# Kernel tuning notes

Hardware: AMD Instinct MI355X
Metric: run time of the kernel (lower is better)

The kernel has to match this reference:

```python
import jax, jax.numpy as jnp
import numpy as np

MESSAGE_PASSES = 3  # constants.message_passes
F_NODE = 64   # hidden_node_features
F_EDGE = 16   # n_edge_features
M_MSG = 64    # message_size
OUT_DIM = 128
B, N = 8, 256
EDGE_DENSITY = 0.1


def setup_inputs() -> dict:
    key = jax.random.key(0)
    ks = jax.random.split(key, 12)
    nodes = jax.random.normal(ks[0], (B, N, F_NODE), dtype=jnp.float32)
    # sparse positive edge features: rand * bernoulli connectivity (avg degree ~ N*density)
    raw = jax.random.uniform(ks[1], (B, N, N, F_EDGE), dtype=jnp.float32)
    conn = (jax.random.uniform(ks[2], (B, N, N)) < EDGE_DENSITY).astype(jnp.float32)
    edges = raw * conn[..., None]
    s = 0.05
    return {
        "nodes": nodes,
        "edges": edges,
        # message MLP: cat(neighbour, edge) -> message_size
        "W_msg": jax.random.normal(ks[3], (F_NODE + F_EDGE, M_MSG), dtype=jnp.float32) * s,
        "b_msg": jnp.zeros((M_MSG,), dtype=jnp.float32),
        # GRU cell (input=message_size, hidden=F_NODE), gates [r|z|n]
        "W_i": jax.random.normal(ks[4], (M_MSG, 3 * F_NODE), dtype=jnp.float32) * s,
        "W_h": jax.random.normal(ks[5], (F_NODE, 3 * F_NODE), dtype=jnp.float32) * s,
        "b_i": jnp.zeros((3 * F_NODE,), dtype=jnp.float32),
        "b_h": jnp.zeros((3 * F_NODE,), dtype=jnp.float32),
        # gated readout
        "W_g": jax.random.normal(ks[6], (2 * F_NODE, OUT_DIM), dtype=jnp.float32) * s,
        "b_g": jnp.zeros((OUT_DIM,), dtype=jnp.float32),
        "W_e": jax.random.normal(ks[7], (F_NODE, OUT_DIM), dtype=jnp.float32) * s,
        "b_e": jnp.zeros((OUT_DIM,), dtype=jnp.float32),
    }


def reference(nodes, edges, W_msg, b_msg, W_i, W_h, b_i, b_h, W_g, b_g, W_e, b_e):
    # adjacency[b,i,j] != 0  <=>  edge (i<-j) exists (original: edges.sum(3).nonzero)
    adjacency = edges.sum(axis=-1)                                   # (B,N,N)
    nbr_mask = (adjacency != 0).astype(nodes.dtype)                  # (B,N,N)
    node_mask = (adjacency.sum(axis=-1) != 0)                        # (B,N) bool
    node_mask_f = node_mask.astype(nodes.dtype)

    h = nodes                                                        # hidden_nodes init = nodes
    b, n, f = nodes.shape
    for _ in range(MESSAGE_PASSES):
        # message_terms over all (node i, neighbour j) pairs; masked sum == padded-gather sum
        nghb = jnp.broadcast_to(h[:, None, :, :], (b, n, n, f))      # (B,N,N,F) neighbour feats
        feat = jnp.concatenate([nghb, edges], axis=-1)               # (B,N,N,F+E)
        terms = jax.nn.relu(feat @ W_msg + b_msg)                    # (B,N,N,M)
        messages = jnp.einsum('bijm,bij->bim', terms, nbr_mask)      # summation aggregation
        # GRU cell update
        gi = messages @ W_i + b_i                                    # (B,N,3F)
        gh = h @ W_h + b_h
        ir, iz, inn = jnp.split(gi, 3, axis=-1)
        hr, hz, hn = jnp.split(gh, 3, axis=-1)
        r = jax.nn.sigmoid(ir + hr)
        z = jax.nn.sigmoid(iz + hz)
        ng = jnp.tanh(inn + r * hn)
        h_new = (1.0 - z) * ng + z * h
        # only nodes with nonzero degree are scattered back (original indexes node_batch idc)
        h = jnp.where(node_mask[..., None], h_new, h)

    # gated readout: sum_i mask_i * sigmoid(g([h_i, x_i])) * e(h_i)
    gate = jax.nn.sigmoid(jnp.concatenate([h, nodes], axis=-1) @ W_g + b_g)  # (B,N,OUT)
    emb = h @ W_e + b_e                                                      # (B,N,OUT)
    out = jnp.einsum('bno,bn->bo', gate * emb, node_mask_f)                  # (B,OUT)
    return out
```

## Files before the change

### kernel.cpp

```cpp
#include <hip/hip_runtime.h>
#include <hip/hip_bf16.h>

#define BB 8
#define NN 256
#define FF 64
#define EE 16
#define MM 64
#define G3 192
#define OUTD 128
#define ROWS (BB*NN)
#define MAXD 64

__device__ __forceinline__ float sigmoidf_(float x) {
    return 1.0f / (1.0f + __expf(-x));
}

__global__ __launch_bounds__(256) void k_prep(
    const float* __restrict__ nodes, const float* __restrict__ edges,
    const float* __restrict__ Wmsg, const float* __restrict__ bmsg,
    int* __restrict__ deg, int* __restrict__ nbr,
    float* __restrict__ h, float* __restrict__ hn)
{
    int row = blockIdx.x;
    int tid = threadIdx.x;
    int lane = tid & 63, wv = tid >> 6;
    __shared__ int wcnt[4];
    __shared__ float snode[FF];

    const float4* ep = (const float4*)(edges + (((size_t)row) * NN + tid) * EE);
    float4 a = ep[0], b4 = ep[1], c4 = ep[2], d4 = ep[3];
    float s = a.x + a.y + a.z + a.w + b4.x + b4.y + b4.z + b4.w
            + c4.x + c4.y + c4.z + c4.w + d4.x + d4.y + d4.z + d4.w;
    bool pred = (s != 0.0f);
    unsigned long long m = __ballot(pred);
    if (lane == 0) wcnt[wv] = __popcll(m);
    if (tid < FF) snode[tid] = nodes[(size_t)row * FF + tid];
    __syncthreads();

    int base = 0;
    #pragma unroll
    for (int q = 0; q < 4; ++q) base += (q < wv) ? wcnt[q] : 0;
    int slot = base + __popcll(m & ((1ull << lane) - 1ull));
    if (pred && slot < MAXD) nbr[row * MAXD + slot] = tid;

    if (tid == 0) {
        int tot = wcnt[0] + wcnt[1] + wcnt[2] + wcnt[3];
        deg[row] = (tot < MAXD) ? tot : MAXD;
    }
    if (tid < FF) h[row * FF + tid] = snode[tid];
    if (tid < MM) {
        float acc = bmsg[tid];
        #pragma unroll 8
        for (int k = 0; k < FF; ++k) acc += snode[k] * Wmsg[k * MM + tid];
        hn[row * MM + tid] = acc;
    }
}

__global__ __launch_bounds__(256) void k_pass(
    const float* __restrict__ edges,
    const float* __restrict__ Wmsg, const float* __restrict__ bmsg,
    const float* __restrict__ Wi, const float* __restrict__ Wh,
    const float* __restrict__ bi, const float* __restrict__ bh,
    const float* __restrict__ nodes,
    const float* __restrict__ Wg, const float* __restrict__ bg,
    const float* __restrict__ We, const float* __restrict__ be,
    const int* __restrict__ deg, const int* __restrict__ nbr,
    const float* __restrict__ hn_in, float* __restrict__ hn_out,
    float* __restrict__ h, float* __restrict__ out, int last)
{
    int row = blockIdx.x, b = row >> 8;
    int tid = threadIdx.x;
    int w = tid >> 6, t = tid & 63;

    __shared__ int   snbr[MAXD];
    __shared__ float efeat[MAXD][EE];
    __shared__ float part[4][MM];
    __shared__ float smsg[MM];
    __shared__ float shold[FF];
    __shared__ float sx[FF];
    __shared__ float gI[3][FF], gH[3][FF];
    __shared__ float shnew[FF];
    __shared__ float eo[OUTD];

    int d = deg[row];
    if (tid < d)  snbr[tid]  = nbr[row * MAXD + tid];
    if (tid < FF) shold[tid] = h[row * FF + tid];
    if (last && tid < FF) sx[tid] = nodes[(size_t)row * FF + tid];

    float we[EE];
    #pragma unroll
    for (int k = 0; k < EE; ++k) we[k] = Wmsg[(FF + k) * MM + t];
    __syncthreads();

    for (int s4 = tid; s4 < d * EE; s4 += 256) {
        int slot = s4 >> 4, k = s4 & 15;
        efeat[slot][k] = edges[(((size_t)row) * NN + snbr[slot]) * EE + k];
    }
    __syncthreads();

    float acc = 0.0f;
    for (int s = w; s < d; s += 4) {
        int j = snbr[s];
        float term = hn_in[(((size_t)b) * NN + j) * MM + t];
        #pragma unroll
        for (int k = 0; k < EE; ++k) term += efeat[s][k] * we[k];
        acc += fmaxf(term, 0.0f);
    }
    part[w][t] = acc;
    __syncthreads();
    if (w == 0) smsg[t] = part[0][t] + part[1][t] + part[2][t] + part[3][t];
    __syncthreads();

    if (w < 3) {
        float gi = bi[w * FF + t], gh = bh[w * FF + t];
        #pragma unroll 4
        for (int k = 0; k < FF; ++k) {
            gi += smsg[k]  * Wi[k * G3 + w * FF + t];
            gh += shold[k] * Wh[k * G3 + w * FF + t];
        }
        gI[w][t] = gi; gH[w][t] = gh;
    }
    __syncthreads();

    if (w == 0) {
        float r  = sigmoidf_(gI[0][t] + gH[0][t]);
        float z  = sigmoidf_(gI[1][t] + gH[1][t]);
        float ng = tanhf(gI[2][t] + r * gH[2][t]);
        float hold = shold[t];
        float hnew = (1.0f - z) * ng + z * hold;
        if (d == 0) hnew = hold;
        shnew[t] = hnew;
        h[row * FF + t] = hnew;
    }
    __syncthreads();

    if (!last) {
        float p = 0.0f;
        #pragma unroll
        for (int kk = 0; kk < 16; ++kk) {
            int k = w * 16 + kk;
            p += shnew[k] * Wmsg[k * MM + t];
        }
        part[w][t] = p;
        __syncthreads();
        if (w == 0)
            hn_out[row * MM + t] = bmsg[t] + part[0][t] + part[1][t] + part[2][t] + part[3][t];
    } else {
        int o = tid & 127, half = tid >> 7;
        float g = 0.0f;
        if (half == 1) {
            float e = be[o];
            #pragma unroll 4
            for (int k = 0; k < FF; ++k) e += shnew[k] * We[k * OUTD + o];
            eo[o] = e;
        } else {
            g = bg[o];
            #pragma unroll 4
            for (int k = 0; k < FF; ++k) g += shnew[k] * Wg[k * OUTD + o];
            #pragma unroll 4
            for (int k = 0; k < FF; ++k) g += sx[k] * Wg[(FF + k) * OUTD + o];
        }
        __syncthreads();
        if (half == 0 && d != 0) {
            float val = sigmoidf_(g) * eo[o];
            atomicAdd(&out[b * OUTD + o], val);
        }
    }
}

extern "C" void kernel_launch(void* const* d_in, const int* in_sizes, int n_in,
                              void* d_out, int out_size, void* d_ws, size_t ws_size,
                              hipStream_t stream) {
    const float* nodes = (const float*)d_in[0];
    const float* edges = (const float*)d_in[1];
    const float* Wmsg  = (const float*)d_in[2];
    const float* bmsg  = (const float*)d_in[3];
    const float* Wi    = (const float*)d_in[4];
    const float* Wh    = (const float*)d_in[5];
    const float* bi    = (const float*)d_in[6];
    const float* bh    = (const float*)d_in[7];
    const float* Wg    = (const float*)d_in[8];
    const float* bg    = (const float*)d_in[9];
    const float* We    = (const float*)d_in[10];
    const float* be    = (const float*)d_in[11];
    float* out = (float*)d_out;

    char* ws = (char*)d_ws;
    int*   deg  = (int*)ws;
    int*   nbr  = (int*)(ws + 8192);
    float* h    = (float*)(ws + 8192 + ROWS * MAXD * 4);
    float* hnA  = h   + ROWS * FF;
    float* hnB  = hnA + ROWS * MM;

    hipMemsetAsync(d_out, 0, (size_t)BB * OUTD * sizeof(float), stream);

    k_prep<<<ROWS, 256, 0, stream>>>(nodes, edges, Wmsg, bmsg, deg, nbr, h, hnA);

    k_pass<<<ROWS, 256, 0, stream>>>(edges, Wmsg, bmsg, Wi, Wh, bi, bh,
                                     nodes, Wg, bg, We, be, deg, nbr,
                                     hnA, hnB, h, out, 0);
    k_pass<<<ROWS, 256, 0, stream>>>(edges, Wmsg, bmsg, Wi, Wh, bi, bh,
                                     nodes, Wg, bg, We, be, deg, nbr,
                                     hnB, hnA, h, out, 0);
    k_pass<<<ROWS, 256, 0, stream>>>(edges, Wmsg, bmsg, Wi, Wh, bi, bh,
                                     nodes, Wg, bg, We, be, deg, nbr,
                                     hnA, hnB, h, out, 1);
}
```

Baseline: 156.2 us.

## Fuse prep and all message passes into one cooperative persistent kernel

Replaces the memset plus four launches with a single cooperative kernel that uses grid.sync between message passes. Each block handles four rows and keeps neighbour lists, edge features and hidden state in shared memory across passes, so edges are read once and h no longer round-trips through global memory. The GRU gate matmuls are batched over the four rows, reusing each weight load four times. The cost is lower parallelism (512 blocks), grid-wide barrier overhead, and a cooperative launch that needs every block co-resident. If occupancy is too low the code falls back to the old multi-kernel path.

```diff
diff --git a/kernel.cpp b/kernel.cpp
--- a/kernel.cpp
+++ b/kernel.cpp
@@ -1,5 +1,8 @@
 #include <hip/hip_runtime.h>
 #include <hip/hip_bf16.h>
+#include <hip/hip_cooperative_groups.h>
+
+namespace cg = cooperative_groups;
 
 #define BB 8
 #define NN 256
@@ -10,9 +13,191 @@
 #define OUTD 128
 #define ROWS (BB*NN)
 #define MAXD 64
+#define RPB  4
+#define NBLK (ROWS/RPB)
 
 __device__ __forceinline__ float sigmoidf_(float x) {
     return 1.0f / (1.0f + __expf(-x));
+}
+
+__global__ __launch_bounds__(256, 4) void k_all(
+    const float* __restrict__ nodes, const float* __restrict__ edges,
+    const float* __restrict__ Wmsg, const float* __restrict__ bmsg,
+    const float* __restrict__ Wi,   const float* __restrict__ Wh,
+    const float* __restrict__ bi,   const float* __restrict__ bh,
+    const float* __restrict__ Wg,   const float* __restrict__ bg,
+    const float* __restrict__ We,   const float* __restrict__ be,
+    float* __restrict__ out, float* __restrict__ hnA, float* __restrict__ hnB)
+{
+    cg::grid_group grid = cg::this_grid();
+
+    const int tid  = threadIdx.x;
+    const int lane = tid & 63;
+    const int w    = tid >> 6;
+    const int gr0  = blockIdx.x * RPB;
+    const int b    = gr0 >> 8;
+
+    __shared__ int   snbr[RPB][MAXD];
+    __shared__ int   sdeg[RPB];
+    __shared__ int   wcnt[RPB][4];
+    __shared__ float efeat[RPB][MAXD][EE];
+    __shared__ float sh[RPB][FF];
+    __shared__ float sx[RPB][FF];
+    __shared__ float smsg[RPB][MM];
+    __shared__ float gates[RPB][6][FF];
+    __shared__ float red[RPB][OUTD];
+
+    bool pr[RPB];
+    unsigned long long mb[RPB];
+    #pragma unroll
+    for (int r = 0; r < RPB; ++r) {
+        const float4* ep = (const float4*)(edges + (((size_t)(gr0 + r)) * NN + tid) * EE);
+        float4 a = ep[0], b4 = ep[1], c4 = ep[2], d4 = ep[3];
+        float s = a.x+a.y+a.z+a.w + b4.x+b4.y+b4.z+b4.w
+                + c4.x+c4.y+c4.z+c4.w + d4.x+d4.y+d4.z+d4.w;
+        pr[r] = (s != 0.0f);
+        mb[r] = __ballot(pr[r]);
+        if (lane == 0) wcnt[r][w] = __popcll(mb[r]);
+    }
+    {
+        int r = tid >> 6, k = tid & 63;
+        float v = nodes[(size_t)(gr0 + r) * FF + k];
+        sh[r][k] = v; sx[r][k] = v;
+    }
+    __syncthreads();
+
+    {
+        unsigned long long low = (1ull << lane) - 1ull;
+        #pragma unroll
+        for (int r = 0; r < RPB; ++r) {
+            int base = 0;
+            #pragma unroll
+            for (int q = 0; q < 4; ++q) base += (q < w) ? wcnt[r][q] : 0;
+            int sl = base + __popcll(mb[r] & low);
+            if (pr[r] && sl < MAXD) snbr[r][sl] = tid;
+        }
+        if (tid < RPB) {
+            int tot = wcnt[tid][0] + wcnt[tid][1] + wcnt[tid][2] + wcnt[tid][3];
+            sdeg[tid] = (tot < MAXD) ? tot : MAXD;
+        }
+    }
+    __syncthreads();
+
+    #pragma unroll
+    for (int r = 0; r < RPB; ++r) {
+        int cnt = sdeg[r] * EE;
+        for (int i = tid; i < cnt; i += 256) {
+            int slot = i >> 4, k = i & 15;
+            efeat[r][slot][k] =
+                edges[(((size_t)(gr0 + r)) * NN + snbr[r][slot]) * EE + k];
+        }
+    }
+
+    {
+        int r = tid >> 6, tt = tid & 63;
+        float acc = bmsg[tt];
+        #pragma unroll 8
+        for (int k = 0; k < FF; ++k) acc += sx[r][k] * Wmsg[k * MM + tt];
+        hnA[(size_t)(gr0 + r) * MM + tt] = acc;
+    }
+    if (blockIdx.x == 0) {
+        #pragma unroll
+        for (int i = 0; i < (BB * OUTD) / 256; ++i) out[i * 256 + tid] = 0.0f;
+    }
+
+    float we[EE];
+    #pragma unroll
+    for (int k = 0; k < EE; ++k) we[k] = Wmsg[(FF + k) * MM + lane];
+
+    grid.sync();
+
+    for (int p = 0; p < 3; ++p) {
+        const float* __restrict__ hin  = (p & 1) ? hnB : hnA;
+        float*       __restrict__ hout = (p & 1) ? hnA : hnB;
+
+        {
+            int d = sdeg[w];
+            const float* hb = hin + (size_t)b * NN * MM;
+            float acc = 0.0f;
+            for (int s = 0; s < d; ++s) {
+                int j = snbr[w][s];
+                float term = hb[j * MM + lane];
+                #pragma unroll
+                for (int k = 0; k < EE; ++k) term += efeat[w][s][k] * we[k];
+                acc += fmaxf(term, 0.0f);
+            }
+            smsg[w][lane] = acc;
+        }
+        __syncthreads();
+
+        for (int q = w; q < 6; q += 4) {
+            float a0, a1, a2, a3;
+            if (q < 3) {
+                a0 = a1 = a2 = a3 = bi[q * FF + lane];
+                #pragma unroll 4
+                for (int k = 0; k < FF; ++k) {
+                    float wgt = Wi[k * G3 + q * FF + lane];
+                    a0 += smsg[0][k] * wgt; a1 += smsg[1][k] * wgt;
+                    a2 += smsg[2][k] * wgt; a3 += smsg[3][k] * wgt;
+                }
+            } else {
+                int g = q - 3;
+                a0 = a1 = a2 = a3 = bh[g * FF + lane];
+                #pragma unroll 4
+                for (int k = 0; k < FF; ++k) {
+                    float wgt = Wh[k * G3 + g * FF + lane];
+                    a0 += sh[0][k] * wgt; a1 += sh[1][k] * wgt;
+                    a2 += sh[2][k] * wgt; a3 += sh[3][k] * wgt;
+                }
+            }
+            gates[0][q][lane] = a0; gates[1][q][lane] = a1;
+            gates[2][q][lane] = a2; gates[3][q][lane] = a3;
+        }
+        __syncthreads();
+
+        {
+            int r = tid >> 6, tt = tid & 63;
+            float rr = sigmoidf_(gates[r][0][tt] + gates[r][3][tt]);
+            float zz = sigmoidf_(gates[r][1][tt] + gates[r][4][tt]);
+            float ng = tanhf(gates[r][2][tt] + rr * gates[r][5][tt]);
+            float hold = sh[r][tt];
+            float hnew = (1.0f - zz) * ng + zz * hold;
+            if (sdeg[r] == 0) hnew = hold;
+            sh[r][tt] = hnew;
+        }
+        __syncthreads();
+
+        if (p < 2) {
+            int r = tid >> 6, tt = tid & 63;
+            float acc = bmsg[tt];
+            #pragma unroll 8
+            for (int k = 0; k < FF; ++k) acc += sh[r][k] * Wmsg[k * MM + tt];
+            hout[(size_t)(gr0 + r) * MM + tt] = acc;
+            grid.sync();
+        }
+    }
+
+    {
+        int r0 = tid >> 7, o = tid & 127;
+        #pragma unroll
+        for (int rr = 0; rr < RPB; rr += 2) {
+            int r = r0 + rr;
+            float g = bg[o], e = be[o];
+            #pragma unroll 4
+            for (int k = 0; k < FF; ++k) {
+                float hk = sh[r][k];
+                g += hk * Wg[k * OUTD + o];
+                e += hk * We[k * OUTD + o];
+            }
+            #pragma unroll 4
+            for (int k = 0; k < FF; ++k) g += sx[r][k] * Wg[(FF + k) * OUTD + o];
+            red[r][o] = (sdeg[r] != 0) ? sigmoidf_(g) * e : 0.0f;
+        }
+        __syncthreads();
+        if (tid < OUTD)
+            atomicAdd(&out[b * OUTD + tid],
+                      red[0][tid] + red[1][tid] + red[2][tid] + red[3][tid]);
+    }
 }
 
 __global__ __launch_bounds__(256) void k_prep(
@@ -29,8 +214,8 @@
 
     const float4* ep = (const float4*)(edges + (((size_t)row) * NN + tid) * EE);
     float4 a = ep[0], b4 = ep[1], c4 = ep[2], d4 = ep[3];
-    float s = a.x + a.y + a.z + a.w + b4.x + b4.y + b4.z + b4.w
-            + c4.x + c4.y + c4.z + c4.w + d4.x + d4.y + d4.z + d4.w;
+    float s = a.x+a.y+a.z+a.w + b4.x+b4.y+b4.z+b4.w
+            + c4.x+c4.y+c4.z+c4.w + d4.x+d4.y+d4.z+d4.w;
     bool pred = (s != 0.0f);
     unsigned long long m = __ballot(pred);
     if (lane == 0) wcnt[wv] = __popcll(m);
@@ -184,18 +369,33 @@
     const float* We    = (const float*)d_in[10];
     const float* be    = (const float*)d_in[11];
     float* out = (float*)d_out;
-
     char* ws = (char*)d_ws;
+
+    int occ = 0;
+    hipError_t qe = hipOccupancyMaxActiveBlocksPerMultiprocessor(
+        &occ, (const void*)k_all, 256, 0);
+    if (qe == hipSuccess && occ * 256 >= NBLK) {
+        float* hnA = (float*)ws;
+        float* hnB = hnA + (size_t)ROWS * MM;
+        void* args[] = {
+            (void*)&nodes, (void*)&edges, (void*)&Wmsg, (void*)&bmsg,
+            (void*)&Wi, (void*)&Wh, (void*)&bi, (void*)&bh,
+            (void*)&Wg, (void*)&bg, (void*)&We, (void*)&be,
+            (void*)&out, (void*)&hnA, (void*)&hnB
+        };
+        hipError_t le = hipLaunchCooperativeKernel(
+            (void*)k_all, dim3(NBLK), dim3(256), args, 0, stream);
+        if (le == hipSuccess) return;
+    }
+
     int*   deg  = (int*)ws;
     int*   nbr  = (int*)(ws + 8192);
-    float* h    = (float*)(ws + 8192 + ROWS * MAXD * 4);
-    float* hnA  = h   + ROWS * FF;
-    float* hnB  = hnA + ROWS * MM;
+    float* h    = (float*)(ws + 8192 + (size_t)ROWS * MAXD * 4);
+    float* hnA  = h   + (size_t)ROWS * FF;
+    float* hnB  = hnA + (size_t)ROWS * MM;
 
     hipMemsetAsync(d_out, 0, (size_t)BB * OUTD * sizeof(float), stream);
-
     k_prep<<<ROWS, 256, 0, stream>>>(nodes, edges, Wmsg, bmsg, deg, nbr, h, hnA);
-
     k_pass<<<ROWS, 256, 0, stream>>>(edges, Wmsg, bmsg, Wi, Wh, bi, bh,
                                      nodes, Wg, bg, We, be, deg, nbr,
                                      hnA, hnB, h, out, 0);
```

After: 334.6 us. 114% more time.

## Process two rows per block in pass kernel and fold output zeroing into prep

Applied to the files above, without the earlier changes.

The per-pass kernel now handles two node rows per 512-thread block. Each GRU and readout weight load is reused for both rows, and the input and hidden gate matvecs run on separate waves instead of one wave doing both. The final readout combines the two rows before a single atomic add, which halves the atomics. The output memset is folded into the prep kernel, removing one launch. The cost is half as many blocks, more shared memory per block, and an unconditional load of 64 neighbour indices per row.

```diff
diff --git a/kernel.cpp b/kernel.cpp
--- a/kernel.cpp
+++ b/kernel.cpp
@@ -19,7 +19,7 @@
     const float* __restrict__ nodes, const float* __restrict__ edges,
     const float* __restrict__ Wmsg, const float* __restrict__ bmsg,
     int* __restrict__ deg, int* __restrict__ nbr,
-    float* __restrict__ h, float* __restrict__ hn)
+    float* __restrict__ h, float* __restrict__ hn, float* __restrict__ out)
 {
     int row = blockIdx.x;
     int tid = threadIdx.x;
@@ -29,8 +29,8 @@
 
     const float4* ep = (const float4*)(edges + (((size_t)row) * NN + tid) * EE);
     float4 a = ep[0], b4 = ep[1], c4 = ep[2], d4 = ep[3];
-    float s = a.x + a.y + a.z + a.w + b4.x + b4.y + b4.z + b4.w
-            + c4.x + c4.y + c4.z + c4.w + d4.x + d4.y + d4.z + d4.w;
+    float s = a.x+a.y+a.z+a.w + b4.x+b4.y+b4.z+b4.w
+            + c4.x+c4.y+c4.z+c4.w + d4.x+d4.y+d4.z+d4.w;
     bool pred = (s != 0.0f);
     unsigned long long m = __ballot(pred);
     if (lane == 0) wcnt[wv] = __popcll(m);
@@ -54,9 +54,13 @@
         for (int k = 0; k < FF; ++k) acc += snode[k] * Wmsg[k * MM + tid];
         hn[row * MM + tid] = acc;
     }
-}
-
-__global__ __launch_bounds__(256) void k_pass(
+    if (row == 0) {
+        #pragma unroll
+        for (int i = 0; i < (BB * OUTD) / 256; ++i) out[i * 256 + tid] = 0.0f;
+    }
+}
+
+__global__ __launch_bounds__(512, 8) void k_pass2(
     const float* __restrict__ edges,
     const float* __restrict__ Wmsg, const float* __restrict__ bmsg,
     const float* __restrict__ Wi, const float* __restrict__ Wh,
@@ -68,102 +72,147 @@
     const float* __restrict__ hn_in, float* __restrict__ hn_out,
     float* __restrict__ h, float* __restrict__ out, int last)
 {
-    int row = blockIdx.x, b = row >> 8;
-    int tid = threadIdx.x;
-    int w = tid >> 6, t = tid & 63;
-
-    __shared__ int   snbr[MAXD];
-    __shared__ float efeat[MAXD][EE];
-    __shared__ float part[4][MM];
-    __shared__ float smsg[MM];
-    __shared__ float shold[FF];
-    __shared__ float sx[FF];
-    __shared__ float gI[3][FF], gH[3][FF];
-    __shared__ float shnew[FF];
-    __shared__ float eo[OUTD];
-
-    int d = deg[row];
-    if (tid < d)  snbr[tid]  = nbr[row * MAXD + tid];
-    if (tid < FF) shold[tid] = h[row * FF + tid];
-    if (last && tid < FF) sx[tid] = nodes[(size_t)row * FF + tid];
+    const int r0  = blockIdx.x * 2;
+    const int b   = r0 >> 8;
+    const int tid = threadIdx.x;
+    const int w   = tid >> 6;
+    const int lane = tid & 63;
+
+    __shared__ int   snbr[2][MAXD];
+    __shared__ int   sdeg[2];
+    __shared__ float efeat[2][MAXD][EE];
+    __shared__ float part[8][MM];
+    __shared__ float smsg[2][MM];
+    __shared__ float shold[2][FF];
+    __shared__ float sx[2][FF];
+    __shared__ float gI[2][3][FF], gH[2][3][FF];
+    __shared__ float shnew[2][FF];
+    __shared__ float sg[2][OUTD], se[2][OUTD];
+
+    if (tid < 2) sdeg[tid] = deg[r0 + tid];
+    if (tid < 2 * MAXD) {
+        int r = tid >> 6;
+        snbr[r][tid & 63] = nbr[(r0 + r) * MAXD + (tid & 63)];
+    }
+    if (tid < 2 * FF) {
+        int r = tid >> 6;
+        shold[r][tid & 63] = h[(size_t)(r0 + r) * FF + (tid & 63)];
+    }
+    if (last && tid >= 2 * FF && tid < 4 * FF) {
+        int r = (tid >> 6) & 1;
+        sx[r][tid & 63] = nodes[(size_t)(r0 + r) * FF + (tid & 63)];
+    }
 
     float we[EE];
     #pragma unroll
-    for (int k = 0; k < EE; ++k) we[k] = Wmsg[(FF + k) * MM + t];
-    __syncthreads();
-
-    for (int s4 = tid; s4 < d * EE; s4 += 256) {
-        int slot = s4 >> 4, k = s4 & 15;
-        efeat[slot][k] = edges[(((size_t)row) * NN + snbr[slot]) * EE + k];
-    }
-    __syncthreads();
-
-    float acc = 0.0f;
-    for (int s = w; s < d; s += 4) {
-        int j = snbr[s];
-        float term = hn_in[(((size_t)b) * NN + j) * MM + t];
-        #pragma unroll
-        for (int k = 0; k < EE; ++k) term += efeat[s][k] * we[k];
-        acc += fmaxf(term, 0.0f);
-    }
-    part[w][t] = acc;
-    __syncthreads();
-    if (w == 0) smsg[t] = part[0][t] + part[1][t] + part[2][t] + part[3][t];
+    for (int k = 0; k < EE; ++k) we[k] = Wmsg[(FF + k) * MM + lane];
+    __syncthreads();
+
+    #pragma unroll
+    for (int r = 0; r < 2; ++r) {
+        int cnt = sdeg[r] * EE;
+        for (int i = tid; i < cnt; i += 512) {
+            int slot = i >> 4, k = i & 15;
+            efeat[r][slot][k] = edges[(((size_t)(r0 + r)) * NN + snbr[r][slot]) * EE + k];
+        }
+    }
+    __syncthreads();
+
+    {
+        int r = w >> 2, sub = w & 3;
+        int d = sdeg[r];
+        const float* hb = hn_in + (size_t)b * NN * MM;
+        float acc = 0.0f;
+        for (int s = sub; s < d; s += 4) {
+            int j = snbr[r][s];
+            float term = hb[j * MM + lane];
+            #pragma unroll
+            for (int k = 0; k < EE; ++k) term += efeat[r][s][k] * we[k];
+            acc += fmaxf(term, 0.0f);
+        }
+        part[w][lane] = acc;
+    }
+    __syncthreads();
+    if ((w & 3) == 0) {
+        int r = w >> 2;
+        smsg[r][lane] = part[w][lane] + part[w + 1][lane]
+                      + part[w + 2][lane] + part[w + 3][lane];
+    }
     __syncthreads();
 
     if (w < 3) {
-        float gi = bi[w * FF + t], gh = bh[w * FF + t];
+        float a0 = bi[w * FF + lane], a1 = a0;
         #pragma unroll 4
         for (int k = 0; k < FF; ++k) {
-            gi += smsg[k]  * Wi[k * G3 + w * FF + t];
-            gh += shold[k] * Wh[k * G3 + w * FF + t];
-        }
-        gI[w][t] = gi; gH[w][t] = gh;
-    }
-    __syncthreads();
-
-    if (w == 0) {
-        float r  = sigmoidf_(gI[0][t] + gH[0][t]);
-        float z  = sigmoidf_(gI[1][t] + gH[1][t]);
-        float ng = tanhf(gI[2][t] + r * gH[2][t]);
-        float hold = shold[t];
-        float hnew = (1.0f - z) * ng + z * hold;
-        if (d == 0) hnew = hold;
-        shnew[t] = hnew;
-        h[row * FF + t] = hnew;
+            float wgt = Wi[k * G3 + w * FF + lane];
+            a0 += smsg[0][k] * wgt;
+            a1 += smsg[1][k] * wgt;
+        }
+        gI[0][w][lane] = a0; gI[1][w][lane] = a1;
+    } else if (w < 6) {
+        int g = w - 3;
+        float a0 = bh[g * FF + lane], a1 = a0;
+        #pragma unroll 4
+        for (int k = 0; k < FF; ++k) {
+            float wgt = Wh[k * G3 + g * FF + lane];
+            a0 += shold[0][k] * wgt;
+            a1 += shold[1][k] * wgt;
+        }
+        gH[0][g][lane] = a0; gH[1][g][lane] = a1;
+    }
+    __syncthreads();
+
+    if (tid < 2 * FF) {
+        int r = tid >> 6, tt = tid & 63;
+        float rr = sigmoidf_(gI[r][0][tt] + gH[r][0][tt]);
+        float zz = sigmoidf_(gI[r][1][tt] + gH[r][1][tt]);
+        float ng = tanhf(gI[r][2][tt] + rr * gH[r][2][tt]);
+        float hold = shold[r][tt];
+        float hnew = (1.0f - zz) * ng + zz * hold;
+        if (sdeg[r] == 0) hnew = hold;
+        shnew[r][tt] = hnew;
+        h[(size_t)(r0 + r) * FF + tt] = hnew;
     }
     __syncthreads();
 
     if (!last) {
-        float p = 0.0f;
-        #pragma unroll
-        for (int kk = 0; kk < 16; ++kk) {
-            int k = w * 16 + kk;
-            p += shnew[k] * Wmsg[k * MM + t];
-        }
-        part[w][t] = p;
+        {
+            int r = w >> 2, kq = w & 3;
+            float p = 0.0f;
+            #pragma unroll
+            for (int kk = 0; kk < 16; ++kk) {
+                int k = kq * 16 + kk;
+                p += shnew[r][k] * Wmsg[k * MM + lane];
+            }
+            part[w][lane] = p;
+        }
         __syncthreads();
-        if (w == 0)
-            hn_out[row * MM + t] = bmsg[t] + part[0][t] + part[1][t] + part[2][t] + part[3][t];
+        if (tid < 2 * MM) {
+            int r = tid >> 6, tt = tid & 63;
+            hn_out[(size_t)(r0 + r) * MM + tt] = bmsg[tt]
+                + part[r*4+0][tt] + part[r*4+1][tt] + part[r*4+2][tt] + part[r*4+3][tt];
+        }
     } else {
-        int o = tid & 127, half = tid >> 7;
-        float g = 0.0f;
-        if (half == 1) {
+        int grp = tid >> 7, o = tid & 127;
+        int r = grp >> 1, kind = grp & 1;
+        if (kind == 0) {
+            float g = bg[o];
+            #pragma unroll 4
+            for (int k = 0; k < FF; ++k) g += shnew[r][k] * Wg[k * OUTD + o];
+            #pragma unroll 4
+            for (int k = 0; k < FF; ++k) g += sx[r][k] * Wg[(FF + k) * OUTD + o];
+            sg[r][o] = g;
+        } else {
             float e = be[o];
             #pragma unroll 4
-            for (int k = 0; k < FF; ++k) e += shnew[k] * We[k * OUTD + o];
-            eo[o] = e;
-        } else {
-            g = bg[o];
-            #pragma unroll 4
-            for (int k = 0; k < FF; ++k) g += shnew[k] * Wg[k * OUTD + o];
-            #pragma unroll 4
-            for (int k = 0; k < FF; ++k) g += sx[k] * Wg[(FF + k) * OUTD + o];
+            for (int k = 0; k < FF; ++k) e += shnew[r][k] * We[k * OUTD + o];
+            se[r][o] = e;
         }
         __syncthreads();
-        if (half == 0 && d != 0) {
-            float val = sigmoidf_(g) * eo[o];
-            atomicAdd(&out[b * OUTD + o], val);
+        if (tid < OUTD) {
+            float v0 = (sdeg[0] != 0) ? sigmoidf_(sg[0][tid]) * se[0][tid] : 0.0f;
+            float v1 = (sdeg[1] != 0) ? sigmoidf_(sg[1][tid]) * se[1][tid] : 0.0f;
+            atomicAdd(&out[b * OUTD + tid], v0 + v1);
         }
     }
 }
@@ -184,25 +233,23 @@
     const float* We    = (const float*)d_in[10];
     const float* be    = (const float*)d_in[11];
     float* out = (float*)d_out;
-
     char* ws = (char*)d_ws;
+
     int*   deg  = (int*)ws;
     int*   nbr  = (int*)(ws + 8192);
-    float* h    = (float*)(ws + 8192 + ROWS * MAXD * 4);
-    float* hnA  = h   + ROWS * FF;
-    float* hnB  = hnA + ROWS * MM;
-
-    hipMemsetAsync(d_out, 0, (size_t)BB * OUTD * sizeof(float), stream);
-
-    k_prep<<<ROWS, 256, 0, stream>>>(nodes, edges, Wmsg, bmsg, deg, nbr, h, hnA);
-
-    k_pass<<<ROWS, 256, 0, stream>>>(edges, Wmsg, bmsg, Wi, Wh, bi, bh,
-                                     nodes, Wg, bg, We, be, deg, nbr,
-                                     hnA, hnB, h, out, 0);
-    k_pass<<<ROWS, 256, 0, stream>>>(edges, Wmsg, bmsg, Wi, Wh, bi, bh,
-                                     nodes, Wg, bg, We, be, deg, nbr,
-                                     hnB, hnA, h, out, 0);
-    k_pass<<<ROWS, 256, 0, stream>>>(edges, Wmsg, bmsg, Wi, Wh, bi, bh,
-                                     nodes, Wg, bg, We, be, deg, nbr,
-                                     hnA, hnB, h, out, 1);
-}
+    float* h    = (float*)(ws + 8192 + (size_t)ROWS * MAXD * 4);
+    float* hnA  = h   + (size_t)ROWS * FF;
+    float* hnB  = hnA + (size_t)ROWS * MM;
+
+    k_prep<<<ROWS, 256, 0, stream>>>(nodes, edges, Wmsg, bmsg, deg, nbr, h, hnA, out);
+
+    k_pass2<<<ROWS/2, 512, 0, stream>>>(edges, Wmsg, bmsg, Wi, Wh, bi, bh,
+                                        nodes, Wg, bg, We, be, deg, nbr,
+                                        hnA, hnB, h, out, 0);
+    k_pass2<<<ROWS/2, 512, 0, stream>>>(edges, Wmsg, bmsg, Wi, Wh, bi, bh,
+                                        nodes, Wg, bg, We, be, deg, nbr,
+                                        hnB, hnA, h, out, 0);
+    k_pass2<<<ROWS/2, 512, 0, stream>>>(edges, Wmsg, bmsg, Wi, Wh, bi, bh,
+                                        nodes, Wg, bg, We, be, deg, nbr,
+                                        hnA, hnB, h, out, 1);
+}
```

After: 144.5 us. -7.5%, faster.
